# Optimization experiments

Hardware: AMD Instinct MI355X
Metric: run time of the kernel (lower is better)

Reference implementation:

```python
import jax, jax.numpy as jnp
import numpy as np

N_NODES = 100000
N_EDGES = 1000000
C_IN, C_HID, C_OUT = 128, 64, 32


def _gcn_layer(x, W, b, src, dst, n):
    """PyG GCNConv with default add_self_loops=True, symmetric normalization.

    x: [N, in], W: [in, out], b: [out], src/dst: [E] int
    """
    h = x @ W  # [N, out] -- transform before aggregation
    # degree of each node counting the added self loop
    deg = jax.ops.segment_sum(jnp.ones_like(dst, dtype=h.dtype), dst, num_segments=n) + 1.0
    dinv = jax.lax.rsqrt(deg)  # deg >= 1 so always finite
    norm = dinv[src] * dinv[dst]  # [E]
    msg = h[src] * norm[:, None]  # [E, out]
    agg = jax.ops.segment_sum(msg, dst, num_segments=n)  # [N, out]
    # self-loop contribution: norm_ii = dinv_i * dinv_i
    out = agg + h * (dinv * dinv)[:, None]
    return out + b


def setup_inputs() -> dict:
    key = jax.random.key(0)
    k1, k2, k3, k4 = jax.random.split(key, 4)
    x = jax.random.normal(k1, (N_NODES, C_IN), dtype=jnp.float32)
    edge_index = jax.random.randint(k2, (2, N_EDGES), 0, N_NODES, dtype=jnp.int64)
    # Glorot-style init for the two GCN layers
    W1 = jax.random.normal(k3, (C_IN, C_HID), dtype=jnp.float32) / np.sqrt(C_IN)
    b1 = jnp.zeros((C_HID,), dtype=jnp.float32)
    W2 = jax.random.normal(k4, (C_HID, C_OUT), dtype=jnp.float32) / np.sqrt(C_HID)
    b2 = jnp.zeros((C_OUT,), dtype=jnp.float32)
    return {"x": x, "edge_index": edge_index, "W1": W1, "b1": b1, "W2": W2, "b2": b2}


def reference(x, edge_index, W1, b1, W2, b2):
    src, dst = edge_index[0], edge_index[1]
    n = x.shape[0]
    h = _gcn_layer(x, W1, b1, src, dst, n)
    h = jax.nn.relu(h)  # Dropout(0.1) is identity in eval mode
    out = _gcn_layer(h, W2, b2, src, dst, n)
    return out
```

## Files before the change

### kernel.cpp

```cpp
#include <hip/hip_runtime.h>
#include <hip/hip_fp16.h>

#define N_NODES 100000
#define N_EDGES 1000000
#define C_IN 128
#define C_HID 64
#define C_OUT 32
#define NB1 ((N_NODES + 255) / 256)
#define GT_BLOCKS ((N_NODES + 63) / 64)
#define AGG1_BLOCKS 6250

__global__ __launch_bounds__(64) void k_detect(const unsigned int* __restrict__ ei,
                                               int* __restrict__ flag) {
    if (threadIdx.x == 0 && blockIdx.x == 0) {
        int is64 = 1;
        for (int i = 0; i < 64; ++i)
            if (ei[2 * i + 1] != 0u) { is64 = 0; break; }
        *flag = is64;
    }
}

__global__ __launch_bounds__(256) void k_rank(const unsigned int* __restrict__ ei,
                                              const int* __restrict__ flag,
                                              int* __restrict__ deg,
                                              int* __restrict__ rank) {
    const int T = gridDim.x * 256;
    const int t = blockIdx.x * 256 + threadIdx.x;
    const bool is64 = (*flag != 0);
    int d[4];
#pragma unroll
    for (int i = 0; i < 4; ++i) {
        int e = t + i * T;
        if (e < N_EDGES)
            d[i] = is64 ? ((const int2*)ei)[(size_t)N_EDGES + e].x
                        : (int)ei[(size_t)N_EDGES + e];
    }
    int r[4];
#pragma unroll
    for (int i = 0; i < 4; ++i) {
        int e = t + i * T;
        if (e < N_EDGES) r[i] = atomicAdd(&deg[d[i]], 1);
    }
#pragma unroll
    for (int i = 0; i < 4; ++i) {
        int e = t + i * T;
        if (e < N_EDGES) __builtin_nontemporal_store(r[i], &rank[e]);
    }
}

__global__ __launch_bounds__(256) void k_scan1(const int* __restrict__ deg,
                                               int* __restrict__ rowstart,
                                               int* __restrict__ blksum,
                                               float* __restrict__ dinv) {
    __shared__ int sm[256];
    int i = blockIdx.x * 256 + threadIdx.x;
    int v = (i < N_NODES) ? deg[i] : 0;
    if (i < N_NODES) dinv[i] = rsqrtf((float)v + 1.0f);
    sm[threadIdx.x] = v;
    __syncthreads();
    for (int o = 1; o < 256; o <<= 1) {
        int t = (threadIdx.x >= o) ? sm[threadIdx.x - o] : 0;
        __syncthreads();
        sm[threadIdx.x] += t;
        __syncthreads();
    }
    if (i < N_NODES) rowstart[i] = sm[threadIdx.x] - v;
    if (threadIdx.x == 255) blksum[blockIdx.x] = sm[255];
}

__global__ __launch_bounds__(512) void k_scan2(const int* __restrict__ blksum,
                                               int* __restrict__ blkoff) {
    __shared__ int sm[512];
    int v = (threadIdx.x < NB1) ? blksum[threadIdx.x] : 0;
    sm[threadIdx.x] = v;
    __syncthreads();
    for (int o = 1; o < 512; o <<= 1) {
        int t = (threadIdx.x >= o) ? sm[threadIdx.x - o] : 0;
        __syncthreads();
        sm[threadIdx.x] += t;
        __syncthreads();
    }
    if (threadIdx.x < NB1) blkoff[threadIdx.x] = sm[threadIdx.x] - v;
}

__global__ __launch_bounds__(256) void k_scan3(int* __restrict__ rowstart,
                                               const int* __restrict__ blkoff) {
    int i = blockIdx.x * 256 + threadIdx.x;
    if (i < N_NODES) rowstart[i] += blkoff[i >> 8];
    if (i == 0) rowstart[N_NODES] = N_EDGES;
}

__global__ __launch_bounds__(256) void k_fill2(const unsigned int* __restrict__ ei,
                                               const int* __restrict__ flag,
                                               const int* __restrict__ rowstart,
                                               const int* __restrict__ rank,
                                               int* __restrict__ esrc) {
    const int T = gridDim.x * 256;
    const int t = blockIdx.x * 256 + threadIdx.x;
    const bool is64 = (*flag != 0);
#pragma unroll
    for (int i = 0; i < 4; ++i) {
        int e = t + i * T;
        if (e < N_EDGES) {
            int s, d;
            if (is64) {
                s = ((const int2*)ei)[e].x;
                d = ((const int2*)ei)[(size_t)N_EDGES + e].x;
            } else {
                s = (int)ei[e];
                d = (int)ei[(size_t)N_EDGES + e];
            }
            int p = rowstart[d] + rank[e];
            __builtin_nontemporal_store(s, &esrc[p]);
        }
    }
}

__global__ __launch_bounds__(256) void k_gemm1(const float* __restrict__ x,
                                               const float* __restrict__ W1,
                                               const float* __restrict__ dinv,
                                               __half* __restrict__ hs1h) {
    __shared__ float w[C_IN * C_HID];
    __shared__ float xt[64 * C_IN];
    const int t = threadIdx.x;
    {
        const float4* W4 = (const float4*)W1;
        const float4* x4g = (const float4*)x;
        float4* w4 = (float4*)w;
        float4* xt4w = (float4*)xt;
        const size_t base = (size_t)blockIdx.x * 64 * (C_IN / 4);
        const size_t xmax = (size_t)N_NODES * (C_IN / 4) - 1;
#pragma unroll
        for (int j = 0; j < 8; ++j) {
            size_t idx = base + t + j * 256;
            if (idx > xmax) idx = xmax;
            xt4w[t + j * 256] = x4g[idx];
            w4[t + j * 256] = W4[t + j * 256];
        }
    }
    __syncthreads();
    const int c2 = t & 31;
    const int h  = (t >> 5) & 1;
    const int wid = t >> 6;
    const int lrow0 = wid * 16 + h * 8;
    const int grow0 = blockIdx.x * 64 + lrow0;
    const float4* xt4 = (const float4*)xt;

    float acc0[8] = {0, 0, 0, 0, 0, 0, 0, 0};
    float acc1[8] = {0, 0, 0, 0, 0, 0, 0, 0};
#pragma unroll 2
    for (int k4 = 0; k4 < C_IN / 4; ++k4) {
        float4 xv[8];
#pragma unroll
        for (int r = 0; r < 8; ++r)
            xv[r] = xt4[(lrow0 + r) * (C_IN / 4) + k4];
        float2 wv[4];
#pragma unroll
        for (int j = 0; j < 4; ++j)
            wv[j] = *reinterpret_cast<const float2*>(&w[(k4 * 4 + j) * C_HID + 2 * c2]);
#pragma unroll
        for (int r = 0; r < 8; ++r) {
            acc0[r] = fmaf(xv[r].x, wv[0].x, acc0[r]);
            acc1[r] = fmaf(xv[r].x, wv[0].y, acc1[r]);
            acc0[r] = fmaf(xv[r].y, wv[1].x, acc0[r]);
            acc1[r] = fmaf(xv[r].y, wv[1].y, acc1[r]);
            acc0[r] = fmaf(xv[r].z, wv[2].x, acc0[r]);
            acc1[r] = fmaf(xv[r].z, wv[2].y, acc1[r]);
            acc0[r] = fmaf(xv[r].w, wv[3].x, acc0[r]);
            acc1[r] = fmaf(xv[r].w, wv[3].y, acc1[r]);
        }
    }
    __half2* h2o = (__half2*)hs1h;
#pragma unroll
    for (int r = 0; r < 8; ++r) {
        int rr = grow0 + r;
        if (rr < N_NODES) {
            float dv = dinv[rr];
            h2o[(size_t)rr * 32 + c2] = __floats2half2_rn(acc0[r] * dv, acc1[r] * dv);
        }
    }
}

__global__ __launch_bounds__(256) void k_agg1g2(const int* __restrict__ rowstart,
                                                const int* __restrict__ esrc,
                                                const __half* __restrict__ hs1h,
                                                const float* __restrict__ dinv,
                                                const float* __restrict__ b1,
                                                const float* __restrict__ W2,
                                                __half* __restrict__ hs2h) {
    __shared__ float2 yrow[4][32];
    const int wid = threadIdx.x >> 6;
    const int lane = threadIdx.x & 63;
    const int c2 = lane & 31;
    const int eo = lane >> 5;
    float Wreg[32];
#pragma unroll
    for (int kk = 0; kk < 16; ++kk) {
        Wreg[2 * kk]     = W2[(32 * eo + 2 * kk) * C_OUT + c2];
        Wreg[2 * kk + 1] = W2[(32 * eo + 2 * kk + 1) * C_OUT + c2];
    }
    const __half2* h2 = (const __half2*)hs1h;
    const float2 bb = { b1[2 * c2], b1[2 * c2 + 1] };
    const int waveId = blockIdx.x * 4 + wid;

    for (int node = waveId; node < N_NODES; node += AGG1_BLOCKS * 4) {
        const int beg = rowstart[node], end = rowstart[node + 1];
        float2 acc; acc.x = 0.f; acc.y = 0.f;
        for (int j0 = beg; j0 < end; j0 += 16) {
            const int jj = j0 + eo;
            int idx[8];
#pragma unroll
            for (int s = 0; s < 8; ++s) {
                int j = jj + 2 * s;
                idx[s] = esrc[j < end ? j : beg];
            }
            float2 v[8];
#pragma unroll
            for (int s = 0; s < 8; ++s)
                v[s] = __half22float2(h2[(size_t)idx[s] * 32 + c2]);
#pragma unroll
            for (int s = 0; s < 8; ++s) {
                if (jj + 2 * s < end) { acc.x += v[s].x; acc.y += v[s].y; }
            }
        }
        acc.x += __shfl_xor(acc.x, 32);
        acc.y += __shfl_xor(acc.y, 32);
        const float dv = dinv[node];
        float2 self = __half22float2(h2[(size_t)node * 32 + c2]);
        float2 y;
        y.x = fmaxf(fmaf(dv, acc.x + self.x, bb.x), 0.f);
        y.y = fmaxf(fmaf(dv, acc.y + self.y, bb.y), 0.f);
        yrow[wid][c2] = y;
        __builtin_amdgcn_wave_barrier();
        float o = 0.f;
#pragma unroll
        for (int kk = 0; kk < 16; ++kk) {
            float2 yv = yrow[wid][16 * eo + kk];
            o = fmaf(yv.x, Wreg[2 * kk], o);
            o = fmaf(yv.y, Wreg[2 * kk + 1], o);
        }
        __builtin_amdgcn_wave_barrier();
        o += __shfl_xor(o, 32);
        if (eo == 0)
            hs2h[(size_t)node * C_OUT + c2] = __float2half(o * dv);
    }
}

__global__ __launch_bounds__(256) void k_agg2(const int* __restrict__ rowstart,
                                              const int* __restrict__ esrc,
                                              const __half* __restrict__ hs2h,
                                              const float* __restrict__ dinv,
                                              const float* __restrict__ b2,
                                              float* __restrict__ out) {
    const int node = blockIdx.x * 4 + (threadIdx.x >> 6);
    const int lane = threadIdx.x & 63;
    const int c2 = lane & 15;
    const int eo = lane >> 4;
    const __half2* h2 = (const __half2*)hs2h;
    const int beg = rowstart[node], end = rowstart[node + 1];
    float2 acc; acc.x = 0.f; acc.y = 0.f;
    for (int j0 = beg; j0 < end; j0 += 16) {
        const int jj = j0 + eo;
        int idx[4];
#pragma unroll
        for (int s = 0; s < 4; ++s) {
            int j = jj + 4 * s;
            idx[s] = esrc[j < end ? j : beg];
        }
        float2 v[4];
#pragma unroll
        for (int s = 0; s < 4; ++s)
            v[s] = __half22float2(h2[(size_t)idx[s] * 16 + c2]);
#pragma unroll
        for (int s = 0; s < 4; ++s) {
            if (jj + 4 * s < end) { acc.x += v[s].x; acc.y += v[s].y; }
        }
    }
    acc.x += __shfl_xor(acc.x, 16);
    acc.y += __shfl_xor(acc.y, 16);
    acc.x += __shfl_xor(acc.x, 32);
    acc.y += __shfl_xor(acc.y, 32);
    if (eo == 0) {
        float2 self = __half22float2(h2[(size_t)node * 16 + c2]);
        float dv = dinv[node];
        float2 o;
        o.x = fmaf(dv, acc.x + self.x, b2[2 * c2]);
        o.y = fmaf(dv, acc.y + self.y, b2[2 * c2 + 1]);
        reinterpret_cast<float2*>(out)[(size_t)node * 16 + c2] = o;
    }
}

extern "C" void kernel_launch(void* const* d_in, const int* in_sizes, int n_in,
                              void* d_out, int out_size, void* d_ws, size_t ws_size,
                              hipStream_t stream) {
    const float* x  = (const float*)d_in[0];
    const unsigned int* ei = (const unsigned int*)d_in[1];
    const float* W1 = (const float*)d_in[2];
    const float* b1 = (const float*)d_in[3];
    const float* W2 = (const float*)d_in[4];
    const float* b2 = (const float*)d_in[5];
    float* out = (float*)d_out;

    char* ws = (char*)d_ws;
    size_t off = 0;
    auto take = [&](size_t bytes) {
        char* p = ws + off;
        off += (bytes + 255) & ~(size_t)255;
        return p;
    };
    int*    flag     = (int*)   take(256);
    int*    esrc     = (int*)   take((size_t)N_EDGES * 4);
    int*    rank     = (int*)   take((size_t)N_EDGES * 4);
    int*    deg      = (int*)   take((size_t)N_NODES * 4);
    int*    rowstart = (int*)   take((size_t)(N_NODES + 1) * 4);
    int*    blksum   = (int*)   take((size_t)NB1 * 4);
    int*    blkoff   = (int*)   take((size_t)NB1 * 4);
    float*  dinv     = (float*) take((size_t)N_NODES * 4);
    __half* hs1h     = (__half*)take((size_t)N_NODES * C_HID * 2);
    __half* hs2h     = (__half*)take((size_t)N_NODES * C_OUT * 2);

    k_detect<<<1, 64, 0, stream>>>(ei, flag);
    hipMemsetAsync(deg, 0, (size_t)N_NODES * 4, stream);
    k_rank<<<1024, 256, 0, stream>>>(ei, flag, deg, rank);

    k_scan1<<<NB1, 256, 0, stream>>>(deg, rowstart, blksum, dinv);
    k_scan2<<<1, 512, 0, stream>>>(blksum, blkoff);
    k_scan3<<<NB1, 256, 0, stream>>>(rowstart, blkoff);

    k_fill2<<<1024, 256, 0, stream>>>(ei, flag, rowstart, rank, esrc);

    k_gemm1<<<GT_BLOCKS, 256, 0, stream>>>(x, W1, dinv, hs1h);

    k_agg1g2<<<AGG1_BLOCKS, 256, 0, stream>>>(rowstart, esrc, hs1h, dinv, b1, W2, hs2h);

    k_agg2<<<N_NODES / 4, 256, 0, stream>>>(rowstart, esrc, hs2h, dinv, b2, out);
}
```

Baseline: 291.8 us.

## Fuse degree counting with first GEMM in one interleaved grid, move dinv scaling to aggregation

The degree/rank atomic pass and the x@W1 GEMM are merged into one launch. Blocks are interleaved so that one in three does edge counting and the rest do GEMM tiles, letting the two independent stages overlap on the device. Since the GEMM now runs before dinv exists, the per-source dinv scaling moves into the layer-1 aggregation as an extra gathered load per edge. The separate detect kernel is dropped in favour of an inline wave-vote check, and W1 is read straight from global memory instead of being staged in shared memory, which lowers LDS use but adds scattered dinv gathers and uncached W reads.

```diff
diff --git a/kernel.cpp b/kernel.cpp
--- a/kernel.cpp
+++ b/kernel.cpp
@@ -7,44 +7,101 @@
 #define C_HID 64
 #define C_OUT 32
 #define NB1 ((N_NODES + 255) / 256)
-#define GT_BLOCKS ((N_NODES + 63) / 64)
+#define GT_BLOCKS 1563
+#define RG_RANK_BLOCKS 781
+#define RG_GRID 2344
 #define AGG1_BLOCKS 6250
 
-__global__ __launch_bounds__(64) void k_detect(const unsigned int* __restrict__ ei,
-                                               int* __restrict__ flag) {
-    if (threadIdx.x == 0 && blockIdx.x == 0) {
-        int is64 = 1;
-        for (int i = 0; i < 64; ++i)
-            if (ei[2 * i + 1] != 0u) { is64 = 0; break; }
-        *flag = is64;
-    }
-}
-
-__global__ __launch_bounds__(256) void k_rank(const unsigned int* __restrict__ ei,
-                                              const int* __restrict__ flag,
-                                              int* __restrict__ deg,
-                                              int* __restrict__ rank) {
-    const int T = gridDim.x * 256;
-    const int t = blockIdx.x * 256 + threadIdx.x;
-    const bool is64 = (*flag != 0);
-    int d[4];
-#pragma unroll
-    for (int i = 0; i < 4; ++i) {
-        int e = t + i * T;
-        if (e < N_EDGES)
-            d[i] = is64 ? ((const int2*)ei)[(size_t)N_EDGES + e].x
-                        : (int)ei[(size_t)N_EDGES + e];
-    }
-    int r[4];
-#pragma unroll
-    for (int i = 0; i < 4; ++i) {
-        int e = t + i * T;
-        if (e < N_EDGES) r[i] = atomicAdd(&deg[d[i]], 1);
-    }
-#pragma unroll
-    for (int i = 0; i < 4; ++i) {
-        int e = t + i * T;
-        if (e < N_EDGES) __builtin_nontemporal_store(r[i], &rank[e]);
+__global__ __launch_bounds__(256) void k_rg1(const unsigned int* __restrict__ ei,
+                                             int* __restrict__ deg,
+                                             int* __restrict__ rank,
+                                             const float* __restrict__ x,
+                                             const float* __restrict__ W1,
+                                             __half* __restrict__ hs1h) {
+    __shared__ float xt[64 * C_IN];
+    const int bid = blockIdx.x;
+    const int m = bid % 3;
+    const int r = bid / 3;
+
+    if (m == 2) {
+        const bool is64 = __all(ei[2 * (threadIdx.x & 63) + 1] == 0u);
+        const int T = RG_RANK_BLOCKS * 256;
+        const int t = r * 256 + threadIdx.x;
+        int d[6];
+#pragma unroll
+        for (int i = 0; i < 6; ++i) {
+            int e = t + i * T;
+            if (e < N_EDGES)
+                d[i] = is64 ? ((const int2*)ei)[(size_t)N_EDGES + e].x
+                            : (int)ei[(size_t)N_EDGES + e];
+        }
+        int rk[6];
+#pragma unroll
+        for (int i = 0; i < 6; ++i) {
+            int e = t + i * T;
+            if (e < N_EDGES) rk[i] = atomicAdd(&deg[d[i]], 1);
+        }
+#pragma unroll
+        for (int i = 0; i < 6; ++i) {
+            int e = t + i * T;
+            if (e < N_EDGES) __builtin_nontemporal_store(rk[i], &rank[e]);
+        }
+        return;
+    }
+
+    const int tile = 2 * r + m;
+    if (tile >= GT_BLOCKS) return;
+    const int t = threadIdx.x;
+    {
+        const float4* x4g = (const float4*)x;
+        float4* xt4w = (float4*)xt;
+        const size_t base = (size_t)tile * 64 * (C_IN / 4);
+        const size_t xmax = (size_t)N_NODES * (C_IN / 4) - 1;
+#pragma unroll
+        for (int j = 0; j < 8; ++j) {
+            size_t idx = base + t + j * 256;
+            if (idx > xmax) idx = xmax;
+            xt4w[t + j * 256] = x4g[idx];
+        }
+    }
+    __syncthreads();
+    const int c2 = t & 31;
+    const int h  = (t >> 5) & 1;
+    const int wid = t >> 6;
+    const int lrow0 = wid * 16 + h * 8;
+    const int grow0 = tile * 64 + lrow0;
+    const float4* xt4 = (const float4*)xt;
+
+    float acc0[8] = {0, 0, 0, 0, 0, 0, 0, 0};
+    float acc1[8] = {0, 0, 0, 0, 0, 0, 0, 0};
+#pragma unroll 2
+    for (int k4 = 0; k4 < C_IN / 4; ++k4) {
+        float4 xv[8];
+#pragma unroll
+        for (int rr = 0; rr < 8; ++rr)
+            xv[rr] = xt4[(lrow0 + rr) * (C_IN / 4) + k4];
+        float2 wv[4];
+#pragma unroll
+        for (int j = 0; j < 4; ++j)
+            wv[j] = *reinterpret_cast<const float2*>(&W1[(k4 * 4 + j) * C_HID + 2 * c2]);
+#pragma unroll
+        for (int rr = 0; rr < 8; ++rr) {
+            acc0[rr] = fmaf(xv[rr].x, wv[0].x, acc0[rr]);
+            acc1[rr] = fmaf(xv[rr].x, wv[0].y, acc1[rr]);
+            acc0[rr] = fmaf(xv[rr].y, wv[1].x, acc0[rr]);
+            acc1[rr] = fmaf(xv[rr].y, wv[1].y, acc1[rr]);
+            acc0[rr] = fmaf(xv[rr].z, wv[2].x, acc0[rr]);
+            acc1[rr] = fmaf(xv[rr].z, wv[2].y, acc1[rr]);
+            acc0[rr] = fmaf(xv[rr].w, wv[3].x, acc0[rr]);
+            acc1[rr] = fmaf(xv[rr].w, wv[3].y, acc1[rr]);
+        }
+    }
+    __half2* h2o = (__half2*)hs1h;
+#pragma unroll
+    for (int rr = 0; rr < 8; ++rr) {
+        int gr = grow0 + rr;
+        if (gr < N_NODES)
+            h2o[(size_t)gr * 32 + c2] = __floats2half2_rn(acc0[rr], acc1[rr]);
     }
 }
 
@@ -91,13 +148,12 @@
 }
 
 __global__ __launch_bounds__(256) void k_fill2(const unsigned int* __restrict__ ei,
-                                               const int* __restrict__ flag,
                                                const int* __restrict__ rowstart,
                                                const int* __restrict__ rank,
                                                int* __restrict__ esrc) {
+    const bool is64 = __all(ei[2 * (threadIdx.x & 63) + 1] == 0u);
     const int T = gridDim.x * 256;
     const int t = blockIdx.x * 256 + threadIdx.x;
-    const bool is64 = (*flag != 0);
 #pragma unroll
     for (int i = 0; i < 4; ++i) {
         int e = t + i * T;
@@ -116,71 +172,6 @@
     }
 }
 
-__global__ __launch_bounds__(256) void k_gemm1(const float* __restrict__ x,
-                                               const float* __restrict__ W1,
-                                               const float* __restrict__ dinv,
-                                               __half* __restrict__ hs1h) {
-    __shared__ float w[C_IN * C_HID];
-    __shared__ float xt[64 * C_IN];
-    const int t = threadIdx.x;
-    {
-        const float4* W4 = (const float4*)W1;
-        const float4* x4g = (const float4*)x;
-        float4* w4 = (float4*)w;
-        float4* xt4w = (float4*)xt;
-        const size_t base = (size_t)blockIdx.x * 64 * (C_IN / 4);
-        const size_t xmax = (size_t)N_NODES * (C_IN / 4) - 1;
-#pragma unroll
-        for (int j = 0; j < 8; ++j) {
-            size_t idx = base + t + j * 256;
-            if (idx > xmax) idx = xmax;
-            xt4w[t + j * 256] = x4g[idx];
-            w4[t + j * 256] = W4[t + j * 256];
-        }
-    }
-    __syncthreads();
-    const int c2 = t & 31;
-    const int h  = (t >> 5) & 1;
-    const int wid = t >> 6;
-    const int lrow0 = wid * 16 + h * 8;
-    const int grow0 = blockIdx.x * 64 + lrow0;
-    const float4* xt4 = (const float4*)xt;
-
-    float acc0[8] = {0, 0, 0, 0, 0, 0, 0, 0};
-    float acc1[8] = {0, 0, 0, 0, 0, 0, 0, 0};
-#pragma unroll 2
-    for (int k4 = 0; k4 < C_IN / 4; ++k4) {
-        float4 xv[8];
-#pragma unroll
-        for (int r = 0; r < 8; ++r)
-            xv[r] = xt4[(lrow0 + r) * (C_IN / 4) + k4];
-        float2 wv[4];
-#pragma unroll
-        for (int j = 0; j < 4; ++j)
-            wv[j] = *reinterpret_cast<const float2*>(&w[(k4 * 4 + j) * C_HID + 2 * c2]);
-#pragma unroll
-        for (int r = 0; r < 8; ++r) {
-            acc0[r] = fmaf(xv[r].x, wv[0].x, acc0[r]);
-            acc1[r] = fmaf(xv[r].x, wv[0].y, acc1[r]);
-            acc0[r] = fmaf(xv[r].y, wv[1].x, acc0[r]);
-            acc1[r] = fmaf(xv[r].y, wv[1].y, acc1[r]);
-            acc0[r] = fmaf(xv[r].z, wv[2].x, acc0[r]);
-            acc1[r] = fmaf(xv[r].z, wv[2].y, acc1[r]);
-            acc0[r] = fmaf(xv[r].w, wv[3].x, acc0[r]);
-            acc1[r] = fmaf(xv[r].w, wv[3].y, acc1[r]);
-        }
-    }
-    __half2* h2o = (__half2*)hs1h;
-#pragma unroll
-    for (int r = 0; r < 8; ++r) {
-        int rr = grow0 + r;
-        if (rr < N_NODES) {
-            float dv = dinv[rr];
-            h2o[(size_t)rr * 32 + c2] = __floats2half2_rn(acc0[r] * dv, acc1[r] * dv);
-        }
-    }
-}
-
 __global__ __launch_bounds__(256) void k_agg1g2(const int* __restrict__ rowstart,
                                                 const int* __restrict__ esrc,
                                                 const __half* __restrict__ hs1h,
@@ -214,13 +205,18 @@
                 int j = jj + 2 * s;
                 idx[s] = esrc[j < end ? j : beg];
             }
+            float ds[8];
+#pragma unroll
+            for (int s = 0; s < 8; ++s)
+                ds[s] = (jj + 2 * s < end) ? dinv[idx[s]] : 0.f;
             float2 v[8];
 #pragma unroll
             for (int s = 0; s < 8; ++s)
                 v[s] = __half22float2(h2[(size_t)idx[s] * 32 + c2]);
 #pragma unroll
             for (int s = 0; s < 8; ++s) {
-                if (jj + 2 * s < end) { acc.x += v[s].x; acc.y += v[s].y; }
+                acc.x = fmaf(ds[s], v[s].x, acc.x);
+                acc.y = fmaf(ds[s], v[s].y, acc.y);
             }
         }
         acc.x += __shfl_xor(acc.x, 32);
@@ -228,8 +224,8 @@
         const float dv = dinv[node];
         float2 self = __half22float2(h2[(size_t)node * 32 + c2]);
         float2 y;
-        y.x = fmaxf(fmaf(dv, acc.x + self.x, bb.x), 0.f);
-        y.y = fmaxf(fmaf(dv, acc.y + self.y, bb.y), 0.f);
+        y.x = fmaxf(fmaf(dv, fmaf(dv, self.x, acc.x), bb.x), 0.f);
+        y.y = fmaxf(fmaf(dv, fmaf(dv, self.y, acc.y), bb.y), 0.f);
         yrow[wid][c2] = y;
         __builtin_amdgcn_wave_barrier();
         float o = 0.f;
@@ -308,7 +304,6 @@
         off += (bytes + 255) & ~(size_t)255;
         return p;
     };
-    int*    flag     = (int*)   take(256);
     int*    esrc     = (int*)   take((size_t)N_EDGES * 4);
     int*    rank     = (int*)   take((size_t)N_EDGES * 4);
     int*    deg      = (int*)   take((size_t)N_NODES * 4);
@@ -319,17 +314,14 @@
     __half* hs1h     = (__half*)take((size_t)N_NODES * C_HID * 2);
     __half* hs2h     = (__half*)take((size_t)N_NODES * C_OUT * 2);
 
-    k_detect<<<1, 64, 0, stream>>>(ei, flag);
     hipMemsetAsync(deg, 0, (size_t)N_NODES * 4, stream);
-    k_rank<<<1024, 256, 0, stream>>>(ei, flag, deg, rank);
+    k_rg1<<<RG_GRID, 256, 0, stream>>>(ei, deg, rank, x, W1, hs1h);
 
     k_scan1<<<NB1, 256, 0, stream>>>(deg, rowstart, blksum, dinv);
     k_scan2<<<1, 512, 0, stream>>>(blksum, blkoff);
     k_scan3<<<NB1, 256, 0, stream>>>(rowstart, blkoff);
 
-    k_fill2<<<1024, 256, 0, stream>>>(ei, flag, rowstart, rank, esrc);
-
-    k_gemm1<<<GT_BLOCKS, 256, 0, stream>>>(x, W1, dinv, hs1h);
+    k_fill2<<<1024, 256, 0, stream>>>(ei, rowstart, rank, esrc);
 
     k_agg1g2<<<AGG1_BLOCKS, 256, 0, stream>>>(rowstart, esrc, hs1h, dinv, b1, W2, hs2h);
 
```

Result: faster. 272.6 us (-6.6%).
